# Performance work log

Hardware: AMD Instinct MI355X
Metric: run time of the kernel (lower is better)

Reference implementation:

```python
import jax, jax.numpy as jnp
import numpy as np


def _conv2d(x, w, b, pad):
    out = jax.lax.conv_general_dilated(
        x, w, window_strides=(1, 1), padding=[(pad, pad), (pad, pad)],
        dimension_numbers=("NCHW", "OIHW", "NCHW"))
    return out + b[None, :, None, None]


def _bilinear_sample(x, py, px):
    # x: [B,C,H,W]; py, px: [B,K,H,W] float sample coords -> [B,C,K,H,W]
    B, C, H, W = x.shape
    y0 = jnp.floor(py)
    x0 = jnp.floor(px)
    y1 = y0 + 1.0
    x1 = x0 + 1.0
    wy1 = py - y0
    wy0 = 1.0 - wy1
    wx1 = px - x0
    wx0 = 1.0 - wx1
    xf = x.reshape(B, C, H * W)

    def corner(yc, xc, wgt):
        valid = (yc >= 0) & (yc <= H - 1) & (xc >= 0) & (xc <= W - 1)
        yi = jnp.clip(yc, 0, H - 1).astype(jnp.int32)
        xi = jnp.clip(xc, 0, W - 1).astype(jnp.int32)
        idx = yi * W + xi                      # [B,K,H,W]
        g = jax.vmap(lambda f, i: f[:, i.reshape(-1)])(xf, idx)  # [B,C,K*H*W]
        g = g.reshape(B, C, idx.shape[1], H, W)
        return g * (wgt * valid)[:, None]      # zero weight outside image

    return (corner(y0, x0, wy0 * wx0) + corner(y0, x1, wy0 * wx1)
            + corner(y1, x0, wy1 * wx0) + corner(y1, x1, wy1 * wx1))


def reference(x, c, w_off, b_off, w_dcn, b_dcn):
    # DCNv2Pack forward: conv_offset(c) -> (o1, o2, mask); modulated deform conv on x.
    B, C, H, W = x.shape
    pad, K = 1, 9
    off_out = _conv2d(c, w_off, b_off, pad)            # [B,27,H,W]
    o1, o2, m = jnp.split(off_out, 3, axis=1)
    offset = jnp.concatenate([o1, o2], axis=1)         # [B,18,H,W]
    mask = jax.nn.sigmoid(m)                           # [B,9,H,W]
    # offset channel layout: [dy_0, dx_0, dy_1, dx_1, ...] per kernel tap
    off = offset.reshape(B, K, 2, H, W)
    ky, kx = jnp.meshgrid(jnp.arange(3), jnp.arange(3), indexing="ij")
    ky = (ky.reshape(K) - pad).astype(x.dtype)
    kx = (kx.reshape(K) - pad).astype(x.dtype)
    base_y = jnp.arange(H, dtype=x.dtype).reshape(1, 1, H, 1)
    base_x = jnp.arange(W, dtype=x.dtype).reshape(1, 1, 1, W)
    py = base_y + ky.reshape(1, K, 1, 1) + off[:, :, 0]  # [B,K,H,W]
    px = base_x + kx.reshape(1, K, 1, 1) + off[:, :, 1]
    samp = _bilinear_sample(x, py, px)                 # [B,C,K,H,W]
    samp = samp * mask[:, None]                        # modulation
    C_out = w_dcn.shape[0]
    out = jnp.einsum("bckhw,ock->bohw", samp, w_dcn.reshape(C_out, C, K))
    return out + b_dcn[None, :, None, None]


def setup_inputs():
    key = jax.random.key(0)
    ks = jax.random.split(key, 4)
    B, C, H, W = 4, 64, 128, 128
    x = jax.random.normal(ks[0], (B, C, H, W), jnp.float32)
    c = jax.random.normal(ks[1], (B, C, H, W), jnp.float32)
    # conv_offset is zero-init in DCNv2Pack; use small random weights so
    # offsets are non-trivial but bounded (realistic trained regime).
    w_off = jax.random.normal(ks[2], (27, C, 3, 3), jnp.float32) * 0.01
    b_off = jnp.zeros((27,), jnp.float32)
    w_dcn = jax.random.normal(ks[3], (C, C, 3, 3), jnp.float32) * (1.0 / np.sqrt(C * 9))
    b_dcn = jnp.zeros((C,), jnp.float32)
    return {"x": x, "c": c, "w_off": w_off, "b_off": b_off,
            "w_dcn": w_dcn, "b_dcn": b_dcn}
```

## Files before the change

kernel.cpp:

```cpp
#include <hip/hip_runtime.h>
#include <math.h>

#define BB 4
#define C 64
#define H 128
#define W 128
#define HW (H*W)
#define KC 576
#define XR 6
#define XC 38

typedef __attribute__((ext_vector_type(4))) float f32x4;
typedef __attribute__((ext_vector_type(8))) _Float16 f16x8;

static __device__ __forceinline__ f16x8 splat8(float f) {
  _Float16 h = (_Float16)f;
  f16x8 v = {h, h, h, h, h, h, h, h};
  return v;
}

__global__ __launch_bounds__(256) void xpose_prep_kernel(
    const float* __restrict__ x, const float* __restrict__ cin,
    const float* __restrict__ wd, const float* __restrict__ woff,
    _Float16* __restrict__ xt, _Float16* __restrict__ ct,
    _Float16* __restrict__ wtbf, _Float16* __restrict__ wotf) {
  __shared__ _Float16 lds16[32 * 72];
  int t = threadIdx.x;

  if (blockIdx.y == 1 && blockIdx.x < 144) {
    int i = blockIdx.x * 256 + t;
    {
      int j = i & 7, ln = (i >> 3) & 63, fi = i >> 9;
      int ot = fi & 3, kb = fi >> 2;
      int o = ot * 16 + (ln & 15);
      int kcol = kb * 32 + (ln >> 4) * 8 + j;
      int k = kcol >> 6, cc = kcol & 63;
      wtbf[i] = (_Float16)wd[(o * C + cc) * 9 + k];
    }
    if (i < 32 * KC) {
      int j = i & 7, ln = (i >> 3) & 63, fi = i >> 9;
      int ot2 = fi & 1, kb = fi >> 1;
      int o = ot2 * 16 + (ln & 15);
      int kcol = kb * 32 + (ln >> 4) * 8 + j;
      int k = kcol >> 6, cc = kcol & 63;
      wotf[i] = (o < 27) ? (_Float16)woff[(o * C + cc) * 9 + k] : (_Float16)0.f;
    }
  }

  const float* src = blockIdx.y ? cin : x;
  _Float16* dst = blockIdx.y ? ct : xt;

  int P0 = blockIdx.x * 32;
  int b = P0 >> 14;
  int pp0 = P0 & (HW - 1);

  int p = t & 31;
  int cg = t >> 5;
  const float* xb = src + (size_t)b * C * HW + pp0 + p;
  f16x8 u;
#pragma unroll
  for (int j = 0; j < 8; ++j)
    u[j] = (_Float16)xb[(cg * 8 + j) * HW];
  *(f16x8*)(lds16 + p * 72 + ((cg ^ (p & 7)) << 3)) = u;

  __syncthreads();

  int q = t >> 3;
  int s = t & 7;
  f16x8 v = *(const f16x8*)(lds16 + q * 72 + ((s ^ (q & 7)) << 3));
  *(f16x8*)(dst + (size_t)(P0 + q) * 64 + s * 8) = v;
}

__global__ __launch_bounds__(256) void dcn_fused_kernel(
    const _Float16* __restrict__ xt, const _Float16* __restrict__ ct,
    const _Float16* __restrict__ wtbf, const _Float16* __restrict__ wotf,
    const float* __restrict__ boff, const float* __restrict__ bd,
    float* __restrict__ out) {
  __shared__ _Float16 win[XR * XC * 64];
  float* offT = (float*)win;

  int tid = threadIdx.x;
  int bid = blockIdx.x;
  int w0 = (bid & 3) * 32;
  int h0 = ((bid >> 2) & 63) * 2;
  int b  = bid >> 8;

  int lane = tid & 63;
  int wv = tid >> 6;
  int lr = lane & 15, lh = lane >> 4;
  int h   = h0 + (wv >> 1);
  int wpx = w0 + (wv & 1) * 16 + lr;

  const _Float16* xtb = xt + (size_t)b * HW * 64;
  const _Float16* ctb = ct + (size_t)b * HW * 64;

  int rlo = min(max(h0 - 2, 0), H - XR);
  int clo = min(max(w0 - 3, 0), W - XC);

  f32x4 acc1a = {0.f, 0.f, 0.f, 0.f};
  f32x4 acc1b = {0.f, 0.f, 0.f, 0.f};
#pragma unroll 2
  for (int kb = 0; kb < 18; ++kb) {
    int t9 = kb >> 1;
    int cg = (kb & 1) * 4 + lh;
    int ty = h + t9 / 3 - 1;
    int tx = wpx + t9 % 3 - 1;
    bool okv = (ty >= 0) && (ty < H) && (tx >= 0) && (tx < W);
    int yc = min(max(ty, 0), H - 1), xc = min(max(tx, 0), W - 1);
    f16x8 bf = *(const f16x8*)(ctb + (size_t)(yc * W + xc) * 64 + cg * 8);
    if (!okv) bf = splat8(0.f);
    f16x8 a0 = *(const f16x8*)(wotf + ((size_t)(kb * 2 + 0) * 64 + lane) * 8);
    f16x8 a1 = *(const f16x8*)(wotf + ((size_t)(kb * 2 + 1) * 64 + lane) * 8);
    acc1a = __builtin_amdgcn_mfma_f32_16x16x32_f16(a0, bf, acc1a, 0, 0, 0);
    acc1b = __builtin_amdgcn_mfma_f32_16x16x32_f16(a1, bf, acc1b, 0, 0, 0);
  }

  {
    f32x4 v0, v1;
#pragma unroll
    for (int r = 0; r < 4; ++r) {
      int o0 = lh * 4 + r;
      int o1 = 16 + lh * 4 + r;
      v0[r] = acc1a[r] + boff[o0];
      v1[r] = acc1b[r] + ((o1 < 27) ? boff[o1] : 0.f);
    }
    *(f32x4*)(offT + ((size_t)wv * 16 + lr) * 36 + lh * 4) = v0;
    *(f32x4*)(offT + ((size_t)wv * 16 + lr) * 36 + 16 + lh * 4) = v1;
  }
  __syncthreads();

  f32x4 rv[7];
#pragma unroll
  for (int j = 0; j < 7; ++j)
    rv[j] = *(const f32x4*)(offT + ((size_t)wv * 16 + lr) * 36 + 4 * j);
  __syncthreads();

#define OFFV(i) (rv[(i) >> 2][(i) & 3])

#pragma unroll
  for (int sweep = 0; sweep < 8; ++sweep) {
    int cch = sweep * 256 + tid;
    if (cch < XR * XC * 8) {
      int row = cch / (XC * 8);
      int rem = cch - row * (XC * 8);
      int col = rem >> 3, part = rem & 7;
      int pix = cch >> 3;
      *(f16x8*)(win + (size_t)pix * 64 + ((part ^ (pix & 7)) << 3)) =
        *(const f16x8*)(xtb + ((size_t)(rlo + row) * W + clo + col) * 64 + part * 8);
    }
  }
  __syncthreads();

  f32x4 acc[4];
#pragma unroll
  for (int i = 0; i < 4; ++i) acc[i] = (f32x4){0.f, 0.f, 0.f, 0.f};

#pragma unroll
  for (int k = 0; k < 9; ++k) {
    float dy = OFFV(2 * k);
    float dx = OFFV(2 * k + 1);
    float mv = OFFV(18 + k);
    float m = 1.0f / (1.0f + __expf(-mv));

    float py = (float)(h + k / 3 - 1) + dy;
    float px = (float)(wpx + k % 3 - 1) + dx;
    float y0f = floorf(py), x0f = floorf(px);
    int y0 = (int)y0f, x0 = (int)x0f;
    float wy1 = py - y0f, wx1 = px - x0f;
    float wy0 = 1.0f - wy1, wx0 = 1.0f - wx1;

    bool y0v = (y0 >= 0) && (y0 < H);
    bool y1v = (y0 + 1 >= 0) && (y0 + 1 < H);
    bool x0v = (x0 >= 0) && (x0 < W);
    bool x1v = (x0 + 1 >= 0) && (x0 + 1 < W);
    int y0c = min(max(y0, 0), H - 1), y1c = min(max(y0 + 1, 0), H - 1);
    int x0c = min(max(x0, 0), W - 1), x1c = min(max(x0 + 1, 0), W - 1);

    float w00 = wy0 * wx0 * (float)(y0v && x0v) * m;
    float w01 = wy0 * wx1 * (float)(y0v && x1v) * m;
    float w10 = wy1 * wx0 * (float)(y1v && x0v) * m;
    float w11 = wy1 * wx1 * (float)(y1v && x1v) * m;

    int iy0 = y0c - rlo, iy1 = y1c - rlo;
    int ix0 = x0c - clo, ix1 = x1c - clo;
    bool inY0 = (unsigned)iy0 < XR, inY1 = (unsigned)iy1 < XR;
    bool inX0 = (unsigned)ix0 < XC, inX1 = (unsigned)ix1 < XC;
    bool in00 = inY0 && inX0, in01 = inY0 && inX1;
    bool in10 = inY1 && inX0, in11 = inY1 && inX1;
    int p00 = min(max(iy0, 0), XR - 1) * XC + min(max(ix0, 0), XC - 1);
    int p01 = min(max(iy0, 0), XR - 1) * XC + min(max(ix1, 0), XC - 1);
    int p10 = min(max(iy1, 0), XR - 1) * XC + min(max(ix0, 0), XC - 1);
    int p11 = min(max(iy1, 0), XR - 1) * XC + min(max(ix1, 0), XC - 1);

#pragma unroll
    for (int half = 0; half < 2; ++half) {
      int cg = half * 4 + lh;
      f16x8 c00 = *(const f16x8*)(win + (size_t)p00 * 64 + ((cg ^ (p00 & 7)) << 3));
      f16x8 c01 = *(const f16x8*)(win + (size_t)p01 * 64 + ((cg ^ (p01 & 7)) << 3));
      f16x8 c10 = *(const f16x8*)(win + (size_t)p10 * 64 + ((cg ^ (p10 & 7)) << 3));
      f16x8 c11 = *(const f16x8*)(win + (size_t)p11 * 64 + ((cg ^ (p11 & 7)) << 3));
      if (!in00) c00 = *(const f16x8*)(xtb + ((size_t)y0c * W + x0c) * 64 + cg * 8);
      if (!in01) c01 = *(const f16x8*)(xtb + ((size_t)y0c * W + x1c) * 64 + cg * 8);
      if (!in10) c10 = *(const f16x8*)(xtb + ((size_t)y1c * W + x0c) * 64 + cg * 8);
      if (!in11) c11 = *(const f16x8*)(xtb + ((size_t)y1c * W + x1c) * 64 + cg * 8);

      f16x8 s = c00 * splat8(w00);
      s += c01 * splat8(w01);
      s += c10 * splat8(w10);
      s += c11 * splat8(w11);

      int kb = 2 * k + half;
#pragma unroll
      for (int ot = 0; ot < 4; ++ot) {
        f16x8 a = *(const f16x8*)(wtbf + ((size_t)(kb * 4 + ot) * 64 + lane) * 8);
        acc[ot] = __builtin_amdgcn_mfma_f32_16x16x32_f16(a, s, acc[ot], 0, 0, 0);
      }
    }
  }

#pragma unroll
  for (int ot = 0; ot < 4; ++ot) {
#pragma unroll
    for (int r = 0; r < 4; ++r) {
      int o = ot * 16 + lh * 4 + r;
      size_t base = ((size_t)(b * C + o)) * HW + (size_t)h * W + w0 + (wv & 1) * 16 + lr;
      out[base] = acc[ot][r] + bd[o];
    }
  }
}

extern "C" void kernel_launch(void* const* d_in, const int* in_sizes, int n_in,
                              void* d_out, int out_size, void* d_ws, size_t ws_size,
                              hipStream_t stream) {
  const float* x    = (const float*)d_in[0];
  const float* c    = (const float*)d_in[1];
  const float* woff = (const float*)d_in[2];
  const float* boff = (const float*)d_in[3];
  const float* wdcn = (const float*)d_in[4];
  const float* bdcn = (const float*)d_in[5];
  float* out = (float*)d_out;

  _Float16* xt   = (_Float16*)d_ws;
  _Float16* ct   = xt + 4194304;
  _Float16* wtbf = ct + 4194304;
  _Float16* wotf = wtbf + 36864;

  int npix = BB * H * W;
  dim3 gx(npix / 32, 2);
  xpose_prep_kernel<<<gx, 256, 0, stream>>>(x, c, wdcn, woff, xt, ct, wtbf, wotf);
  dcn_fused_kernel<<<npix / 64, 256, 0, stream>>>(xt, ct, wtbf, wotf, boff, bdcn, out);
}
```

Baseline: 45.30 us.

## Stage offset-conv input tile in LDS and keep offsets in fp16

The offset convolution now loads the 4x34-pixel tile of the transposed c tensor into shared memory cooperatively. It then reads its nine taps from LDS instead of gathering them from global memory nine times per pixel. The conv results are kept in fp16 in a dedicated LDS region, so they no longer alias the x window. This lets the offset read-back overlap the x-window fill and removes one barrier. The cost is an extra cooperative load phase with its own barrier, plus reduced precision for the sampling offsets and mask logits.

```diff
diff --git a/kernel.cpp b/kernel.cpp
--- a/kernel.cpp
+++ b/kernel.cpp
@@ -9,8 +9,12 @@
 #define KC 576
 #define XR 6
 #define XC 38
+#define CR 4
+#define CCW 34
+#define OFFS 28
 
 typedef __attribute__((ext_vector_type(4))) float f32x4;
+typedef __attribute__((ext_vector_type(4))) _Float16 f16x4;
 typedef __attribute__((ext_vector_type(8))) _Float16 f16x8;
 
 static __device__ __forceinline__ f16x8 splat8(float f) {
@@ -76,8 +80,9 @@
     const _Float16* __restrict__ wtbf, const _Float16* __restrict__ wotf,
     const float* __restrict__ boff, const float* __restrict__ bd,
     float* __restrict__ out) {
-  __shared__ _Float16 win[XR * XC * 64];
-  float* offT = (float*)win;
+  __shared__ __align__(16) unsigned char smem[32768];
+  _Float16* win  = (_Float16*)smem;
+  _Float16* offT = (_Float16*)(smem + 29184);
 
   int tid = threadIdx.x;
   int bid = blockIdx.x;
@@ -94,8 +99,22 @@
   const _Float16* xtb = xt + (size_t)b * HW * 64;
   const _Float16* ctb = ct + (size_t)b * HW * 64;
 
-  int rlo = min(max(h0 - 2, 0), H - XR);
-  int clo = min(max(w0 - 3, 0), W - XC);
+  int crlo = min(max(h0 - 1, 0), H - CR);
+  int cclo = min(max(w0 - 1, 0), W - CCW);
+  int rlo  = min(max(h0 - 2, 0), H - XR);
+  int clo  = min(max(w0 - 3, 0), W - XC);
+
+#pragma unroll
+  for (int sweep = 0; sweep < 5; ++sweep) {
+    int cch = sweep * 256 + tid;
+    if (cch < CR * CCW * 8) {
+      int pixw = cch >> 3, part = cch & 7;
+      int row = pixw / CCW, col = pixw - row * CCW;
+      *(f16x8*)(win + (size_t)pixw * 64 + ((part ^ (pixw & 7)) << 3)) =
+        *(const f16x8*)(ctb + ((size_t)(crlo + row) * W + cclo + col) * 64 + part * 8);
+    }
+  }
+  __syncthreads();
 
   f32x4 acc1a = {0.f, 0.f, 0.f, 0.f};
   f32x4 acc1b = {0.f, 0.f, 0.f, 0.f};
@@ -106,8 +125,9 @@
     int ty = h + t9 / 3 - 1;
     int tx = wpx + t9 % 3 - 1;
     bool okv = (ty >= 0) && (ty < H) && (tx >= 0) && (tx < W);
-    int yc = min(max(ty, 0), H - 1), xc = min(max(tx, 0), W - 1);
-    f16x8 bf = *(const f16x8*)(ctb + (size_t)(yc * W + xc) * 64 + cg * 8);
+    int pixw = (min(max(ty, 0), H - 1) - crlo) * CCW
+             + (min(max(tx, 0), W - 1) - cclo);
+    f16x8 bf = *(const f16x8*)(win + (size_t)pixw * 64 + ((cg ^ (pixw & 7)) << 3));
     if (!okv) bf = splat8(0.f);
     f16x8 a0 = *(const f16x8*)(wotf + ((size_t)(kb * 2 + 0) * 64 + lane) * 8);
     f16x8 a1 = *(const f16x8*)(wotf + ((size_t)(kb * 2 + 1) * 64 + lane) * 8);
@@ -116,40 +136,37 @@
   }
 
   {
-    f32x4 v0, v1;
+    f16x4 v0, v1;
 #pragma unroll
     for (int r = 0; r < 4; ++r) {
       int o0 = lh * 4 + r;
       int o1 = 16 + lh * 4 + r;
-      v0[r] = acc1a[r] + boff[o0];
-      v1[r] = acc1b[r] + ((o1 < 27) ? boff[o1] : 0.f);
-    }
-    *(f32x4*)(offT + ((size_t)wv * 16 + lr) * 36 + lh * 4) = v0;
-    *(f32x4*)(offT + ((size_t)wv * 16 + lr) * 36 + 16 + lh * 4) = v1;
-  }
-  __syncthreads();
-
-  f32x4 rv[7];
-#pragma unroll
-  for (int j = 0; j < 7; ++j)
-    rv[j] = *(const f32x4*)(offT + ((size_t)wv * 16 + lr) * 36 + 4 * j);
-  __syncthreads();
-
-#define OFFV(i) (rv[(i) >> 2][(i) & 3])
+      v0[r] = (_Float16)(acc1a[r] + boff[o0]);
+      v1[r] = (_Float16)(acc1b[r] + ((o1 < 27) ? boff[o1] : 0.f));
+    }
+    _Float16* base = offT + ((size_t)wv * 16 + lr) * OFFS;
+    *(f16x4*)(base + lh * 4) = v0;
+    if (lh < 3) *(f16x4*)(base + 16 + lh * 4) = v1;
+  }
+  __syncthreads();
 
 #pragma unroll
   for (int sweep = 0; sweep < 8; ++sweep) {
     int cch = sweep * 256 + tid;
     if (cch < XR * XC * 8) {
-      int row = cch / (XC * 8);
-      int rem = cch - row * (XC * 8);
-      int col = rem >> 3, part = rem & 7;
-      int pix = cch >> 3;
-      *(f16x8*)(win + (size_t)pix * 64 + ((part ^ (pix & 7)) << 3)) =
+      int pixw = cch >> 3, part = cch & 7;
+      int row = pixw / XC, col = pixw - row * XC;
+      *(f16x8*)(win + (size_t)pixw * 64 + ((part ^ (pixw & 7)) << 3)) =
         *(const f16x8*)(xtb + ((size_t)(rlo + row) * W + clo + col) * 64 + part * 8);
     }
   }
-  __syncthreads();
+  f16x4 rvh[7];
+#pragma unroll
+  for (int j = 0; j < 7; ++j)
+    rvh[j] = *(const f16x4*)(offT + ((size_t)wv * 16 + lr) * OFFS + 4 * j);
+  __syncthreads();
+
+#define OFFV(i) ((float)rvh[(i) >> 2][(i) & 3])
 
   f32x4 acc[4];
 #pragma unroll
```

New measurement: 39.95 us (median of 2 runs). 1.13x faster.
